# Optimization experiments

Measured on AMD Instinct MI355X. Metric: run time of the kernel, lower is better.

## Reference

```python
import jax, jax.numpy as jnp
import numpy as np

VOCAB = 21
EPS = 1e-5


def rmsnorm(x, w):
    return x * jax.lax.rsqrt(jnp.mean(x * x, axis=-1, keepdims=True) + EPS) * w


def mamba_layer(h, in_w, conv_w, conv_b, xp_w, dtp_w, dtp_b, A_log, Dp, out_w):
    # h: (B, L, D)
    Bsz, L, _ = h.shape
    di, dc = conv_w.shape
    n = A_log.shape[-1]
    r = dtp_w.shape[-1]
    xz = jnp.einsum('bld,ed->ble', h, in_w)          # (B, L, 2*di)
    xi, z = jnp.split(xz, 2, axis=-1)
    # causal depthwise conv of width dc
    xp = jnp.pad(xi, ((0, 0), (dc - 1, 0), (0, 0)))
    xc = conv_b + sum(xp[:, k:k + L, :] * conv_w[:, k] for k in range(dc))
    xc = jax.nn.silu(xc)                              # (B, L, di)
    dbc = jnp.einsum('bld,ed->ble', xc, xp_w)         # (B, L, r+2n)
    dt, Bm, Cm = dbc[..., :r], dbc[..., r:r + n], dbc[..., r + n:]
    dt = jax.nn.softplus(jnp.einsum('blr,dr->bld', dt, dtp_w) + dtp_b)  # (B, L, di)
    A = -jnp.exp(A_log)                               # (di, n)

    def step(hst, inp):
        x_t, dt_t, B_t, C_t = inp                     # (B,di),(B,di),(B,n),(B,n)
        dA = jnp.exp(dt_t[..., None] * A)             # (B, di, n)
        hst = dA * hst + (dt_t * x_t)[..., None] * B_t[:, None, :]
        y_t = jnp.einsum('bdn,bn->bd', hst, C_t)
        return hst, y_t

    h0 = jnp.zeros((Bsz, di, n), dtype=h.dtype)
    xs = (xc.swapaxes(0, 1), dt.swapaxes(0, 1), Bm.swapaxes(0, 1), Cm.swapaxes(0, 1))
    _, ys = jax.lax.scan(step, h0, xs)
    y = ys.swapaxes(0, 1) + xc * Dp                   # skip term D*x
    y = y * jax.nn.silu(z)                            # gate
    return jnp.einsum('bld,ed->ble', y, out_w)


def setup_inputs() -> dict:
    key = jax.random.key(0)
    B, L, D = 4, 1024, 512
    n_layers, n, dc, expand = 2, 16, 3, 2
    di = expand * D
    r = (D + 15) // 16  # dt_rank = ceil(d_model/16) = 32
    ks = jax.random.split(key, 12)
    f32 = jnp.float32
    inp = {}
    inp['x'] = jax.random.randint(ks[0], (B, L), 0, VOCAB)
    inp['emb'] = 0.02 * jax.random.normal(ks[1], (VOCAB, D), f32)
    inp['norm_w'] = jnp.ones((n_layers, D), f32)
    inp['in_proj_w'] = (D ** -0.5) * jax.random.normal(ks[2], (n_layers, 2 * di, D), f32)
    inp['conv_w'] = (dc ** -0.5) * jax.random.normal(ks[3], (n_layers, di, dc), f32)
    inp['conv_b'] = jnp.zeros((n_layers, di), f32)
    inp['x_proj_w'] = (di ** -0.5) * jax.random.normal(ks[4], (n_layers, r + 2 * n, di), f32)
    inp['dt_proj_w'] = (r ** -0.5) * jax.random.normal(ks[5], (n_layers, di, r), f32)
    inp['dt_proj_b'] = jax.random.uniform(ks[6], (n_layers, di), f32, minval=-4.0, maxval=-1.0)
    inp['A_log'] = jnp.log(jnp.broadcast_to(jnp.arange(1, n + 1, dtype=f32), (n_layers, di, n)))
    inp['D_param'] = jnp.ones((n_layers, di), f32)
    inp['out_proj_w'] = (di ** -0.5) * jax.random.normal(ks[7], (n_layers, D, di), f32)
    inp['fc_w'] = (D ** -0.5) * jax.random.normal(ks[8], (2, D), f32)
    inp['fc_b'] = jnp.zeros((2,), f32)
    return inp


def reference(x, emb, norm_w, in_proj_w, conv_w, conv_b, x_proj_w, dt_proj_w,
              dt_proj_b, A_log, D_param, out_proj_w, fc_w, fc_b):
    h = emb[x].astype(jnp.float32)                    # (B, L, D)
    n_layers = norm_w.shape[0]
    for l in range(n_layers):
        h = rmsnorm(
            mamba_layer(h, in_proj_w[l], conv_w[l], conv_b[l], x_proj_w[l],
                        dt_proj_w[l], dt_proj_b[l], A_log[l], D_param[l],
                        out_proj_w[l]),
            norm_w[l])
    pooled = jnp.mean(h, axis=1)                      # global_pool=True
    out = jnp.tanh(pooled)                            # dropout is identity at eval
    return out @ fc_w.T + fc_b                        # (B, 2)
```

## Files before the change

### kernel.cpp

```cpp
#include <hip/hip_runtime.h>
#include <math.h>

constexpr int Bsz = 4, Lseq = 1024, Dmodel = 512, NLAYERS = 2;
constexpr int DI = 1024, NST = 16, RNK = 32;
constexpr int BLQ = Bsz * Lseq;
constexpr int NCH = 32, CLEN = 32;

typedef __attribute__((ext_vector_type(8))) short short8v;
typedef __attribute__((ext_vector_type(8))) unsigned short ushort8v;
typedef __attribute__((ext_vector_type(4))) float f32x4;
typedef unsigned short ushort;

__device__ inline ushort bf16_rne(float v) {
  unsigned u = __float_as_uint(v);
  u += 0x7FFFu + ((u >> 16) & 1u);
  return (ushort)(u >> 16);
}
__device__ inline float bf2f(ushort u) {
  return __uint_as_float(((unsigned)u) << 16);
}
__device__ inline size_t frag_off(int row, int k, int KT) {
  int kt = k >> 6, kk = (k >> 5) & 1, k8 = (k >> 3) & 3;
  int lanei = (row & 15) | (k8 << 4), msub = (row >> 4) & 7, rt = row >> 7;
  return ((((size_t)(rt * KT + kt) * 2 + kk) * 8 + msub) * 64 + lanei) * 8;
}
#define GLDS(gp, lp) __builtin_amdgcn_global_load_lds( \
    (const __attribute__((address_space(1))) void*)(gp), \
    (__attribute__((address_space(3))) void*)(lp), 16, 0, 0)

__global__ __launch_bounds__(256) void embed_kernel(const int* __restrict__ x,
    const float* __restrict__ emb, ushort* __restrict__ Af) {
  int i = blockIdx.x * 256 + threadIdx.x;
  int row = i >> 6, k = (i & 63) * 8;
  int tok = x[row];
  const float* src = &emb[(size_t)tok * Dmodel + k];
  float4 v0 = *reinterpret_cast<const float4*>(src);
  float4 v1 = *reinterpret_cast<const float4*>(src + 4);
  float xs[8] = {v0.x, v0.y, v0.z, v0.w, v1.x, v1.y, v1.z, v1.w};
  ushort hv[8];
#pragma unroll
  for (int e = 0; e < 8; ++e) hv[e] = bf16_rne(xs[e]);
  *reinterpret_cast<ushort8v*>(&Af[frag_off(row, k, 8)]) =
      *reinterpret_cast<ushort8v*>(hv);
}

__global__ __launch_bounds__(256) void cvtw_kernel(
    const float* __restrict__ in_w, const float* __restrict__ xp_w,
    const float* __restrict__ out_w, const float* __restrict__ dtp_w,
    ushort* __restrict__ WIh, ushort* __restrict__ WIl,
    ushort* __restrict__ XPh, ushort* __restrict__ XPl,
    ushort* __restrict__ WOh, ushort* __restrict__ WOl,
    ushort* __restrict__ DTWh, ushort* __restrict__ DTWl)
{
  int blk = blockIdx.x;
  const float* src; ushort *dh, *dl; size_t doff;
  if (blk < 1024) {
    int u = blk * 256 + threadIdx.x;
    int l = u >> 17, rem = u & 131071;
    int row = rem >> 6, k = (rem & 63) * 8;
    src = in_w + (size_t)l * 2048 * 512 + (size_t)row * 512 + k;
    size_t base = (size_t)l * 2048 * 512;
    dh = WIh + base; dl = WIl + base; doff = frag_off(row, k, 8);
  } else if (blk < 1088) {
    int u = (blk - 1024) * 256 + threadIdx.x;
    int l = u >> 13, rem = u & 8191;
    int row = rem >> 7, k = (rem & 127) * 8;
    src = xp_w + (size_t)l * 64 * 1024 + (size_t)row * 1024 + k;
    size_t base = (size_t)l * 131072;
    dh = XPh + base; dl = XPl + base; doff = frag_off(row, k, 16);
  } else if (blk < 1600) {
    int u = (blk - 1088) * 256 + threadIdx.x;
    int l = u >> 16, rem = u & 65535;
    int row = rem >> 7, k = (rem & 127) * 8;
    src = out_w + (size_t)l * 512 * 1024 + (size_t)row * 1024 + k;
    size_t base = (size_t)l * 512 * 1024;
    dh = WOh + base; dl = WOl + base; doff = frag_off(row, k, 16);
  } else {
    int u = (blk - 1600) * 256 + threadIdx.x;
    int l = u >> 12, rem = u & 4095;
    int n = rem >> 2, k8 = rem & 3, k = k8 * 8;
    src = dtp_w + (size_t)l * 1024 * 32 + (size_t)n * 32 + k;
    size_t base = (size_t)l * 32768;
    dh = DTWh + base; dl = DTWl + base;
    doff = (size_t)((n >> 4) * 64 + ((n & 15) | (k8 << 4))) * 8;
  }
  float4 v0 = *reinterpret_cast<const float4*>(src);
  float4 v1 = *reinterpret_cast<const float4*>(src + 4);
  float xs[8] = {v0.x, v0.y, v0.z, v0.w, v1.x, v1.y, v1.z, v1.w};
  ushort hs[8], ls[8];
#pragma unroll
  for (int j = 0; j < 8; ++j) {
    unsigned u = __float_as_uint(xs[j]);
    float hf = __uint_as_float(u & 0xFFFF0000u);
    float r = xs[j] - hf;
    hs[j] = (ushort)(u >> 16);
    ls[j] = (ushort)(__float_as_uint(r) >> 16);
  }
  *reinterpret_cast<ushort8v*>(&dh[doff]) = *reinterpret_cast<ushort8v*>(hs);
  *reinterpret_cast<ushort8v*>(&dl[doff]) = *reinterpret_cast<ushort8v*>(ls);
}

template<int OB>
__global__ __launch_bounds__(256) void gemm_mfma(
    const ushort* __restrict__ Ah,
    const ushort* __restrict__ Bh, const ushort* __restrict__ Bl,
    void* __restrict__ Cv, int N, int K)
{
  const int KT = K >> 6;
  constexpr int ASZ = 2 * 8 * 64 * 8;
  __shared__ ushort lds[3 * ASZ];
  const int tid = threadIdx.x;
  const int lane = tid & 63, wid = tid >> 6;
  const int wm = wid >> 1, wn = wid & 1;
  const int bm0 = blockIdx.y * 128, bn0 = blockIdx.x * 128;
  const size_t abase = (size_t)blockIdx.y * KT * ASZ;
  const size_t bbase = (size_t)blockIdx.x * KT * ASZ;
  const ushort* gsrc = (wid == 0) ? Ah : (wid == 1) ? Bh : Bl;
  const size_t gb = (wid == 0) ? abase : bbase;
  f32x4 acc[4][4];
#pragma unroll
  for (int i = 0; i < 4; ++i)
#pragma unroll
    for (int j = 0; j < 4; ++j) acc[i][j] = (f32x4){0.f, 0.f, 0.f, 0.f};
  const int msel = wm * 4, nsel = wn * 4;
  for (int kt = 0; kt < KT; ++kt) {
    if (wid < 3) {
      const ushort* sbase = gsrc + gb + (size_t)kt * ASZ + lane * 8;
#pragma unroll
      for (int i = 0; i < 16; ++i)
        GLDS(sbase + i * 512, lds + wid * ASZ + i * 512);
    }
    __syncthreads();
#pragma unroll
    for (int kk = 0; kk < 2; ++kk) {
      short8v a_h[4], b_h[4], b_l[4];
#pragma unroll
      for (int i = 0; i < 4; ++i) {
        int ai = ((kk * 8 + msel + i) * 64 + lane) * 8;
        int bi = ((kk * 8 + nsel + i) * 64 + lane) * 8;
        a_h[i] = *reinterpret_cast<const short8v*>(&lds[0 * ASZ + ai]);
        b_h[i] = *reinterpret_cast<const short8v*>(&lds[1 * ASZ + bi]);
        b_l[i] = *reinterpret_cast<const short8v*>(&lds[2 * ASZ + bi]);
      }
#pragma unroll
      for (int ms = 0; ms < 4; ++ms)
#pragma unroll
        for (int ns = 0; ns < 4; ++ns) {
          acc[ms][ns] = __builtin_amdgcn_mfma_f32_16x16x32_bf16(a_h[ms], b_h[ns], acc[ms][ns], 0, 0, 0);
          acc[ms][ns] = __builtin_amdgcn_mfma_f32_16x16x32_bf16(a_h[ms], b_l[ns], acc[ms][ns], 0, 0, 0);
        }
    }
    __syncthreads();
  }
  const int cr = lane >> 4, cc = lane & 15;
#pragma unroll
  for (int ms = 0; ms < 4; ++ms) {
    int row0 = bm0 + (msel + ms) * 16 + cr * 4;
#pragma unroll
    for (int ns = 0; ns < 4; ++ns) {
      int col = bn0 + (nsel + ns) * 16 + cc;
#pragma unroll
      for (int r = 0; r < 4; ++r) {
        if (OB) ((ushort*)Cv)[(size_t)(row0 + r) * N + col] = bf16_rne(acc[ms][ns][r]);
        else    ((float*)Cv)[(size_t)(row0 + r) * N + col] = acc[ms][ns][r];
      }
    }
  }
}

__global__ __launch_bounds__(256) void convxp_kernel(
    const ushort* __restrict__ XZb, const float* __restrict__ cw,
    const float* __restrict__ cb,
    const ushort* __restrict__ XPh, const ushort* __restrict__ XPl,
    const ushort* __restrict__ DTWh, const ushort* __restrict__ DTWl,
    const float* __restrict__ dtb,
    float* __restrict__ XC, float* __restrict__ DTb, float* __restrict__ BCc)
{
  constexpr int XZOFF = 0;
  constexpr int AOFF  = 1312;
  constexpr int BHOFF = 2336;
  constexpr int BLOFF = 6432;
  __shared__ ushort smu[10528];
  const int tid = threadIdx.x, lane = tid & 63, wid = tid >> 6;
  const int cr = lane >> 4, cc = lane & 15;
  const int bm0 = blockIdx.x * 16;
  const int batchbase = bm0 & ~(Lseq - 1);
  f32x4 acc = (f32x4){0.f, 0.f, 0.f, 0.f};

  for (int kt = 0; kt < 16; ++kt) {
    const int kcol0 = kt * 64;
    if (wid < 2) {
#pragma unroll
      for (int i = 0; i < 2; ++i) {
        int u = tid + i * 128;
        if (u < 144) {
          int r = u >> 3, c8 = u & 7;
          int grow = bm0 - 2 + r;
          ushort8v v = {};
          if (grow >= batchbase)
            v = *reinterpret_cast<const ushort8v*>(
                &XZb[(size_t)grow * 2048 + kcol0 + c8 * 8]);
          *reinterpret_cast<ushort8v*>(&smu[XZOFF + r * 72 + c8 * 8]) = v;
        }
      }
    } else {
      const ushort* src = ((wid == 2) ? XPh : XPl) + (size_t)kt * 8192 + lane * 8;
      int dst0 = (wid == 2) ? BHOFF : BLOFF;
#pragma unroll
      for (int i = 0; i < 8; ++i) {
        int sidx = (i >> 2) * 8 + (i & 3);
        int didx = i;
        GLDS(src + sidx * 512, smu + dst0 + didx * 512);
      }
    }
    __syncthreads();
    if (tid < 128) {
      int row = tid >> 3, c8 = tid & 7;
      int d0 = kcol0 + c8 * 8;
      ushort8v cur = *reinterpret_cast<ushort8v*>(&smu[XZOFF + (row + 2) * 72 + c8 * 8]);
      ushort8v pm1 = *reinterpret_cast<ushort8v*>(&smu[XZOFF + (row + 1) * 72 + c8 * 8]);
      ushort8v pm2 = *reinterpret_cast<ushort8v*>(&smu[XZOFF + (row + 0) * 72 + c8 * 8]);
      float wv[24], bv[8];
#pragma unroll
      for (int q = 0; q < 6; ++q)
        *reinterpret_cast<float4*>(&wv[q * 4]) =
            *reinterpret_cast<const float4*>(&cw[d0 * 3 + q * 4]);
      *reinterpret_cast<float4*>(&bv[0]) = *reinterpret_cast<const float4*>(&cb[d0]);
      *reinterpret_cast<float4*>(&bv[4]) = *reinterpret_cast<const float4*>(&cb[d0 + 4]);
      float os[8]; ushort hv[8];
#pragma unroll
      for (int e = 0; e < 8; ++e) {
        float a = bv[e];
        a = fmaf(bf2f(pm2[e]), wv[e * 3 + 0], a);
        a = fmaf(bf2f(pm1[e]), wv[e * 3 + 1], a);
        a = fmaf(bf2f(cur[e]), wv[e * 3 + 2], a);
        float s = a / (1.f + __expf(-a));
        os[e] = s; hv[e] = bf16_rne(s);
      }
      float* op = &XC[(size_t)(bm0 + row) * DI + d0];
      *reinterpret_cast<float4*>(op) = *reinterpret_cast<float4*>(&os[0]);
      *reinterpret_cast<float4*>(op + 4) = *reinterpret_cast<float4*>(&os[4]);
      int kk = c8 >> 2, k8 = c8 & 3;
      int lanei = row | (k8 << 4);
      *reinterpret_cast<ushort8v*>(&smu[AOFF + (kk * 64 + lanei) * 8]) =
          *reinterpret_cast<ushort8v*>(hv);
    }
    __syncthreads();
#pragma unroll
    for (int kk = 0; kk < 2; ++kk) {
      short8v a = *reinterpret_cast<const short8v*>(&smu[AOFF + (kk * 64 + lane) * 8]);
      short8v bh = *reinterpret_cast<const short8v*>(&smu[BHOFF + ((kk * 4 + wid) * 64 + lane) * 8]);
      short8v bl = *reinterpret_cast<const short8v*>(&smu[BLOFF + ((kk * 4 + wid) * 64 + lane) * 8]);
      acc = __builtin_amdgcn_mfma_f32_16x16x32_bf16(a, bh, acc, 0, 0, 0);
      acc = __builtin_amdgcn_mfma_f32_16x16x32_bf16(a, bl, acc, 0, 0, 0);
    }
    __syncthreads();
  }
  if (wid >= 2) {
#pragma unroll
    for (int r = 0; r < 4; ++r)
      BCc[(size_t)(bm0 + cr * 4 + r) * 32 + (wid - 2) * 16 + cc] = acc[r];
  } else {
    int k = wid * 16 + cc, k8 = k >> 3;
#pragma unroll
    for (int r = 0; r < 4; ++r)
      smu[(((cr * 4 + r) | (k8 << 4)) * 8) + (k & 7)] = bf16_rne(acc[r]);
  }
  __syncthreads();
  short8v a_dt = *reinterpret_cast<const short8v*>(&smu[lane * 8]);
#pragma unroll 4
  for (int i = 0; i < 16; ++i) {
    int nt = wid * 16 + i;
    short8v bh = *reinterpret_cast<const short8v*>(&DTWh[(size_t)(nt * 64 + lane) * 8]);
    short8v bl = *reinterpret_cast<const short8v*>(&DTWl[(size_t)(nt * 64 + lane) * 8]);
    f32x4 p = (f32x4){0.f, 0.f, 0.f, 0.f};
    p = __builtin_amdgcn_mfma_f32_16x16x32_bf16(a_dt, bh, p, 0, 0, 0);
    p = __builtin_amdgcn_mfma_f32_16x16x32_bf16(a_dt, bl, p, 0, 0, 0);
    int n = nt * 16 + cc;
    float bias = dtb[n];
#pragma unroll
    for (int r = 0; r < 4; ++r) {
      float v = p[r] + bias;
      float sp = (v > 15.f) ? v : log1pf(__expf(v));
      DTb[(size_t)(bm0 + cr * 4 + r) * DI + n] = sp;
    }
  }
}

__global__ __launch_bounds__(256) void scan_p1_kernel(
    const float* __restrict__ DTb, const float* __restrict__ XC,
    const float* __restrict__ BCc, const float* __restrict__ Alog,
    float* __restrict__ HEND, float* __restrict__ DSUM)
{
  const int d = blockIdx.x * 256 + threadIdx.x;
  const int c = blockIdx.y, b = blockIdx.z;
  const int t0 = b * Lseq + c * CLEN;
  __shared__ float Bs[CLEN][16];
#pragma unroll
  for (int i = 0; i < 2; ++i) {
    int e = threadIdx.x + i * 256;
    Bs[e >> 4][e & 15] = BCc[(size_t)(t0 + (e >> 4)) * 32 + (e & 15)];
  }
  float An[16];
#pragma unroll
  for (int j = 0; j < 4; ++j) {
    float4 a = *reinterpret_cast<const float4*>(&Alog[d * 16 + j * 4]);
    An[j * 4 + 0] = -__expf(a.x); An[j * 4 + 1] = -__expf(a.y);
    An[j * 4 + 2] = -__expf(a.z); An[j * 4 + 3] = -__expf(a.w);
  }
  __syncthreads();
  float h[16] = {};
  float S = 0.f;
  for (int t = 0; t < CLEN; ++t) {
    size_t g = (size_t)(t0 + t) * DI + d;
    float dt = DTb[g], xc = XC[g];
    S += dt;
    float dtxc = dt * xc;
#pragma unroll
    for (int n = 0; n < 16; ++n)
      h[n] = fmaf(__expf(An[n] * dt), h[n], dtxc * Bs[t][n]);
  }
  size_t hb = ((size_t)(b * NCH + c) * DI + d) * 16;
#pragma unroll
  for (int j = 0; j < 4; ++j)
    *reinterpret_cast<float4*>(&HEND[hb + j * 4]) =
        *reinterpret_cast<float4*>(&h[j * 4]);
  DSUM[(size_t)(b * NCH + c) * DI + d] = S;
}

__global__ __launch_bounds__(256) void scan_p2_kernel(
    float* __restrict__ HEND, const float* __restrict__ DSUM,
    const float* __restrict__ Alog)
{
  int id = blockIdx.x * 256 + threadIdx.x;
  int n = id & 15, d = (id >> 4) & (DI - 1), b = id >> 14;
  float An = -__expf(Alog[d * 16 + n]);
  float hg = 0.f;
  for (int c = 0; c < NCH; ++c) {
    size_t hi = ((size_t)(b * NCH + c) * DI + d) * 16 + n;
    float hl = HEND[hi];
    float Dc = DSUM[(size_t)(b * NCH + c) * DI + d];
    HEND[hi] = hg;
    hg = fmaf(__expf(An * Dc), hg, hl);
  }
}

__global__ __launch_bounds__(256) void scan_p3_kernel(
    const float* __restrict__ XC, const float* __restrict__ DTb,
    const float* __restrict__ BCc, const ushort* __restrict__ XZb,
    const float* __restrict__ HEND, const float* __restrict__ Alog,
    const float* __restrict__ Dp, ushort* __restrict__ Af)
{
  const int tid = threadIdx.x;
  const int dg = blockIdx.x, c = blockIdx.y, b = blockIdx.z;
  const int d = dg * 256 + tid;
  const int t0 = b * Lseq + c * CLEN;
  __shared__ float BC[CLEN][32];
  __shared__ float ys[CLEN][264];
#pragma unroll
  for (int i = 0; i < 4; ++i) {
    int e = tid + i * 256;
    BC[e >> 5][e & 31] = BCc[(size_t)(t0 + (e >> 5)) * 32 + (e & 31)];
  }
  float An[16], h[16];
  size_t hb = ((size_t)(b * NCH + c) * DI + d) * 16;
#pragma unroll
  for (int j = 0; j < 4; ++j) {
    float4 a = *reinterpret_cast<const float4*>(&Alog[d * 16 + j * 4]);
    An[j * 4 + 0] = -__expf(a.x); An[j * 4 + 1] = -__expf(a.y);
    An[j * 4 + 2] = -__expf(a.z); An[j * 4 + 3] = -__expf(a.w);
    *reinterpret_cast<float4*>(&h[j * 4]) =
        *reinterpret_cast<const float4*>(&HEND[hb + j * 4]);
  }
  float Dpv = Dp[d];
  __syncthreads();
  for (int t = 0; t < CLEN; ++t) {
    size_t g = (size_t)(t0 + t) * DI + d;
    float dt = DTb[g], xc = XC[g];
    float z = bf2f(XZb[(size_t)(t0 + t) * (2 * DI) + DI + d]);
    float dtxc = dt * xc;
    float y = 0.f;
#pragma unroll
    for (int n = 0; n < 16; ++n) {
      h[n] = fmaf(__expf(An[n] * dt), h[n], dtxc * BC[t][n]);
      y = fmaf(h[n], BC[t][16 + n], y);
    }
    float sil = z / (1.f + __expf(-z));
    ys[t][tid] = (y + xc * Dpv) * sil;
  }
  __syncthreads();
#pragma unroll
  for (int i = 0; i < 4; ++i) {
    int u = tid + i * 256;
    int tt = u >> 5, j8 = u & 31;
    int row = t0 + tt;
    int kg = dg * 256 + j8 * 8;
    ushort hv[8];
#pragma unroll
    for (int e = 0; e < 8; ++e) hv[e] = bf16_rne(ys[tt][j8 * 8 + e]);
    *reinterpret_cast<ushort8v*>(&Af[frag_off(row, kg, 16)]) =
        *reinterpret_cast<ushort8v*>(hv);
  }
}

__global__ __launch_bounds__(256) void rmsnorm_kernel(const float* __restrict__ X,
    const float* __restrict__ W, float* __restrict__ O, ushort* __restrict__ Af) {
  int row = blockIdx.x * 4 + (threadIdx.x >> 6);
  int lane = threadIdx.x & 63;
  int k = lane * 8;
  const float* xp = X + (size_t)row * Dmodel + k;
  float4 v0 = *reinterpret_cast<const float4*>(xp);
  float4 v1 = *reinterpret_cast<const float4*>(xp + 4);
  float vs[8] = {v0.x, v0.y, v0.z, v0.w, v1.x, v1.y, v1.z, v1.w};
  float ss = 0.f;
#pragma unroll
  for (int e = 0; e < 8; ++e) ss = fmaf(vs[e], vs[e], ss);
#pragma unroll
  for (int o = 32; o >= 1; o >>= 1) ss += __shfl_xor(ss, o);
  float sc = rsqrtf(ss * (1.f / Dmodel) + 1e-5f);
  const float* wp = W + k;
  float4 w0 = *reinterpret_cast<const float4*>(wp);
  float4 w1 = *reinterpret_cast<const float4*>(wp + 4);
  float wsv[8] = {w0.x, w0.y, w0.z, w0.w, w1.x, w1.y, w1.z, w1.w};
  float os[8];
  ushort hv[8];
#pragma unroll
  for (int e = 0; e < 8; ++e) {
    os[e] = vs[e] * sc * wsv[e];
    hv[e] = bf16_rne(os[e]);
  }
  float* op = O + (size_t)row * Dmodel + k;
  *reinterpret_cast<float4*>(op) = *reinterpret_cast<float4*>(&os[0]);
  *reinterpret_cast<float4*>(op + 4) = *reinterpret_cast<float4*>(&os[4]);
  *reinterpret_cast<ushort8v*>(&Af[frag_off(row, k, 8)]) =
      *reinterpret_cast<ushort8v*>(hv);
}

__global__ __launch_bounds__(256) void pool_part_kernel(const float* __restrict__ H,
    float* __restrict__ part) {
  int b = blockIdx.x, dg = blockIdx.y, tc = blockIdx.z;
  int tid = threadIdx.x;
  int d = dg * 128 + (tid & 127);
  int ph = tid >> 7;
  const float* base = H + ((size_t)(b * Lseq + tc * 128 + ph * 64)) * Dmodel + d;
  float s = 0.f;
#pragma unroll 8
  for (int t = 0; t < 64; ++t) s += base[(size_t)t * Dmodel];
  __shared__ float red[256];
  red[tid] = s; __syncthreads();
  if (ph == 0)
    part[(size_t)(b * 8 + tc) * Dmodel + d] = red[tid] + red[tid + 128];
}

__global__ __launch_bounds__(256) void pool_head_kernel(
    const float* __restrict__ part, const float* __restrict__ fcw,
    const float* __restrict__ fcb, float* __restrict__ out) {
  int b = blockIdx.x >> 1, j = blockIdx.x & 1;
  int tid = threadIdx.x;
  float s = 0.f;
  for (int d = tid; d < Dmodel; d += 256) {
    float p = 0.f;
#pragma unroll
    for (int tc = 0; tc < 8; ++tc) p += part[(size_t)(b * 8 + tc) * Dmodel + d];
    s += tanhf(p * (1.f / Lseq)) * fcw[j * Dmodel + d];
  }
#pragma unroll
  for (int o = 32; o >= 1; o >>= 1) s += __shfl_xor(s, o);
  __shared__ float w[4];
  if ((tid & 63) == 0) w[tid >> 6] = s;
  __syncthreads();
  if (tid == 0) out[b * 2 + j] = w[0] + w[1] + w[2] + w[3] + fcb[j];
}

extern "C" void kernel_launch(void* const* d_in, const int* in_sizes, int n_in,
                              void* d_out, int out_size, void* d_ws, size_t ws_size,
                              hipStream_t stream) {
  const int*   x      = (const int*)d_in[0];
  const float* emb    = (const float*)d_in[1];
  const float* norm_w = (const float*)d_in[2];
  const float* in_w   = (const float*)d_in[3];
  const float* conv_w = (const float*)d_in[4];
  const float* conv_b = (const float*)d_in[5];
  const float* xp_w   = (const float*)d_in[6];
  const float* dtp_w  = (const float*)d_in[7];
  const float* dtp_b  = (const float*)d_in[8];
  const float* A_log  = (const float*)d_in[9];
  const float* Dp     = (const float*)d_in[10];
  const float* out_w  = (const float*)d_in[11];
  const float* fc_w   = (const float*)d_in[12];
  const float* fc_b   = (const float*)d_in[13];
  float* out = (float*)d_out;

  char* p = (char*)d_ws;
  auto alloc = [&](size_t bytes) { char* r = p; p += (bytes + 255) & ~255ull; return r; };
  ushort* XZb  = (ushort*)alloc((size_t)BLQ * 2 * DI * 2);
  float*  XC   = (float*) alloc((size_t)BLQ * DI * 4);
  float*  DTb  = (float*) alloc((size_t)BLQ * DI * 4);
  float*  BCc  = (float*) alloc((size_t)BLQ * 32 * 4);
  float*  HEND = (float*) alloc((size_t)Bsz * NCH * DI * 16 * 4);
  float*  DSUM = (float*) alloc((size_t)Bsz * NCH * DI * 4);
  float*  H    = (float*) alloc((size_t)BLQ * Dmodel * 4);
  float*  H2   = (float*) alloc((size_t)BLQ * Dmodel * 4);
  float*  PPART= (float*) alloc((size_t)Bsz * 8 * Dmodel * 4);
  ushort* AhI  = (ushort*)alloc((size_t)BLQ * Dmodel * 2);
  ushort* AhO  = (ushort*)alloc((size_t)BLQ * DI * 2);
  ushort* WIh  = (ushort*)alloc((size_t)2 * 2048 * 512 * 2);
  ushort* WIl  = (ushort*)alloc((size_t)2 * 2048 * 512 * 2);
  ushort* XPh  = (ushort*)alloc((size_t)2 * 131072 * 2);
  ushort* XPl  = (ushort*)alloc((size_t)2 * 131072 * 2);
  ushort* WOh  = (ushort*)alloc((size_t)2 * 512 * 1024 * 2);
  ushort* WOl  = (ushort*)alloc((size_t)2 * 512 * 1024 * 2);
  ushort* DTWh = (ushort*)alloc((size_t)2 * 32768 * 2);
  ushort* DTWl = (ushort*)alloc((size_t)2 * 32768 * 2);

  embed_kernel<<<BLQ * Dmodel / 8 / 256, 256, 0, stream>>>(x, emb, AhI);
  cvtw_kernel<<<1632, 256, 0, stream>>>(in_w, xp_w, out_w, dtp_w,
      WIh, WIl, XPh, XPl, WOh, WOl, DTWh, DTWl);

  for (int l = 0; l < NLAYERS; ++l) {
    const float* cw  = conv_w + (size_t)l * DI * 3;
    const float* cb  = conv_b + (size_t)l * DI;
    const float* dtb = dtp_b + (size_t)l * DI;
    const float* Al  = A_log + (size_t)l * DI * NST;
    const float* dpl = Dp    + (size_t)l * DI;
    const float* nw  = norm_w + (size_t)l * Dmodel;
    const ushort* wih = WIh + (size_t)l * 2048 * 512;
    const ushort* wil = WIl + (size_t)l * 2048 * 512;
    const ushort* xph = XPh + (size_t)l * 131072;
    const ushort* xpl = XPl + (size_t)l * 131072;
    const ushort* woh = WOh + (size_t)l * 512 * 1024;
    const ushort* wol = WOl + (size_t)l * 512 * 1024;
    const ushort* dwh = DTWh + (size_t)l * 32768;
    const ushort* dwl = DTWl + (size_t)l * 32768;

    gemm_mfma<1><<<dim3(16, 32), 256, 0, stream>>>(AhI, wih, wil, XZb, 2 * DI, Dmodel);

    convxp_kernel<<<BLQ / 16, 256, 0, stream>>>(XZb, cw, cb, xph, xpl,
        dwh, dwl, dtb, XC, DTb, BCc);

    scan_p1_kernel<<<dim3(DI / 256, NCH, Bsz), 256, 0, stream>>>(
        DTb, XC, BCc, Al, HEND, DSUM);
    scan_p2_kernel<<<Bsz * DI * NST / 256, 256, 0, stream>>>(HEND, DSUM, Al);
    scan_p3_kernel<<<dim3(DI / 256, NCH, Bsz), 256, 0, stream>>>(
        XC, DTb, BCc, XZb, HEND, Al, dpl, AhO);

    gemm_mfma<0><<<dim3(4, 32), 256, 0, stream>>>(AhO, woh, wol, H2, Dmodel, DI);

    rmsnorm_kernel<<<BLQ / 4, 256, 0, stream>>>(H2, nw, H, AhI);
  }

  pool_part_kernel<<<dim3(Bsz, Dmodel / 128, 8), 256, 0, stream>>>(H, PPART);
  pool_head_kernel<<<2 * Bsz, 256, 0, stream>>>(PPART, fc_w, fc_b, out);
}
```

Baseline: 314.6 us.

## Split x_proj K-loop, move dt_proj to fp32 kernel, drop out_proj low-bf16 term

The conv+x_proj kernel now splits its K loop across two grid slices that write fp32 partial sums. A new xpost kernel adds the partials, emits B/C, and computes dt_proj plus softplus in fp32 FMA from LDS instead of bf16 split MFMA. The A-operand LDS writes and reads get an XOR swizzle to cut bank conflicts. The out_proj GEMM drops the low-half weight MFMA, halving its matrix work but lowering the precision of out_proj weights to plain bf16.

```diff
diff --git a/kernel.cpp b/kernel.cpp
--- a/kernel.cpp
+++ b/kernel.cpp
@@ -46,11 +46,10 @@
 
 __global__ __launch_bounds__(256) void cvtw_kernel(
     const float* __restrict__ in_w, const float* __restrict__ xp_w,
-    const float* __restrict__ out_w, const float* __restrict__ dtp_w,
+    const float* __restrict__ out_w,
     ushort* __restrict__ WIh, ushort* __restrict__ WIl,
     ushort* __restrict__ XPh, ushort* __restrict__ XPl,
-    ushort* __restrict__ WOh, ushort* __restrict__ WOl,
-    ushort* __restrict__ DTWh, ushort* __restrict__ DTWl)
+    ushort* __restrict__ WOh, ushort* __restrict__ WOl)
 {
   int blk = blockIdx.x;
   const float* src; ushort *dh, *dl; size_t doff;
@@ -68,21 +67,13 @@
     src = xp_w + (size_t)l * 64 * 1024 + (size_t)row * 1024 + k;
     size_t base = (size_t)l * 131072;
     dh = XPh + base; dl = XPl + base; doff = frag_off(row, k, 16);
-  } else if (blk < 1600) {
+  } else {
     int u = (blk - 1088) * 256 + threadIdx.x;
     int l = u >> 16, rem = u & 65535;
     int row = rem >> 7, k = (rem & 127) * 8;
     src = out_w + (size_t)l * 512 * 1024 + (size_t)row * 1024 + k;
     size_t base = (size_t)l * 512 * 1024;
     dh = WOh + base; dl = WOl + base; doff = frag_off(row, k, 16);
-  } else {
-    int u = (blk - 1600) * 256 + threadIdx.x;
-    int l = u >> 12, rem = u & 4095;
-    int n = rem >> 2, k8 = rem & 3, k = k8 * 8;
-    src = dtp_w + (size_t)l * 1024 * 32 + (size_t)n * 32 + k;
-    size_t base = (size_t)l * 32768;
-    dh = DTWh + base; dl = DTWl + base;
-    doff = (size_t)((n >> 4) * 64 + ((n & 15) | (k8 << 4))) * 8;
   }
   float4 v0 = *reinterpret_cast<const float4*>(src);
   float4 v1 = *reinterpret_cast<const float4*>(src + 4);
@@ -100,7 +91,7 @@
   *reinterpret_cast<ushort8v*>(&dl[doff]) = *reinterpret_cast<ushort8v*>(ls);
 }
 
-template<int OB>
+template<int OB, int SPLITB>
 __global__ __launch_bounds__(256) void gemm_mfma(
     const ushort* __restrict__ Ah,
     const ushort* __restrict__ Bh, const ushort* __restrict__ Bl,
@@ -124,7 +115,7 @@
     for (int j = 0; j < 4; ++j) acc[i][j] = (f32x4){0.f, 0.f, 0.f, 0.f};
   const int msel = wm * 4, nsel = wn * 4;
   for (int kt = 0; kt < KT; ++kt) {
-    if (wid < 3) {
+    if (wid < (SPLITB ? 3 : 2)) {
       const ushort* sbase = gsrc + gb + (size_t)kt * ASZ + lane * 8;
 #pragma unroll
       for (int i = 0; i < 16; ++i)
@@ -140,14 +131,15 @@
         int bi = ((kk * 8 + nsel + i) * 64 + lane) * 8;
         a_h[i] = *reinterpret_cast<const short8v*>(&lds[0 * ASZ + ai]);
         b_h[i] = *reinterpret_cast<const short8v*>(&lds[1 * ASZ + bi]);
-        b_l[i] = *reinterpret_cast<const short8v*>(&lds[2 * ASZ + bi]);
+        if (SPLITB) b_l[i] = *reinterpret_cast<const short8v*>(&lds[2 * ASZ + bi]);
       }
 #pragma unroll
       for (int ms = 0; ms < 4; ++ms)
 #pragma unroll
         for (int ns = 0; ns < 4; ++ns) {
           acc[ms][ns] = __builtin_amdgcn_mfma_f32_16x16x32_bf16(a_h[ms], b_h[ns], acc[ms][ns], 0, 0, 0);
-          acc[ms][ns] = __builtin_amdgcn_mfma_f32_16x16x32_bf16(a_h[ms], b_l[ns], acc[ms][ns], 0, 0, 0);
+          if (SPLITB)
+            acc[ms][ns] = __builtin_amdgcn_mfma_f32_16x16x32_bf16(a_h[ms], b_l[ns], acc[ms][ns], 0, 0, 0);
         }
     }
     __syncthreads();
@@ -172,9 +164,7 @@
     const ushort* __restrict__ XZb, const float* __restrict__ cw,
     const float* __restrict__ cb,
     const ushort* __restrict__ XPh, const ushort* __restrict__ XPl,
-    const ushort* __restrict__ DTWh, const ushort* __restrict__ DTWl,
-    const float* __restrict__ dtb,
-    float* __restrict__ XC, float* __restrict__ DTb, float* __restrict__ BCc)
+    float* __restrict__ XC, float* __restrict__ P)
 {
   constexpr int XZOFF = 0;
   constexpr int AOFF  = 1312;
@@ -184,10 +174,11 @@
   const int tid = threadIdx.x, lane = tid & 63, wid = tid >> 6;
   const int cr = lane >> 4, cc = lane & 15;
   const int bm0 = blockIdx.x * 16;
+  const int z = blockIdx.y;
   const int batchbase = bm0 & ~(Lseq - 1);
   f32x4 acc = (f32x4){0.f, 0.f, 0.f, 0.f};
 
-  for (int kt = 0; kt < 16; ++kt) {
+  for (int kt = z * 8; kt < z * 8 + 8; ++kt) {
     const int kcol0 = kt * 64;
     if (wid < 2) {
 #pragma unroll
@@ -209,8 +200,7 @@
 #pragma unroll
       for (int i = 0; i < 8; ++i) {
         int sidx = (i >> 2) * 8 + (i & 3);
-        int didx = i;
-        GLDS(src + sidx * 512, smu + dst0 + didx * 512);
+        GLDS(src + sidx * 512, smu + dst0 + i * 512);
       }
     }
     __syncthreads();
@@ -241,14 +231,15 @@
       *reinterpret_cast<float4*>(op) = *reinterpret_cast<float4*>(&os[0]);
       *reinterpret_cast<float4*>(op + 4) = *reinterpret_cast<float4*>(&os[4]);
       int kk = c8 >> 2, k8 = c8 & 3;
-      int lanei = row | (k8 << 4);
-      *reinterpret_cast<ushort8v*>(&smu[AOFF + (kk * 64 + lanei) * 8]) =
+      int idx = (kk * 64 + (row | (k8 << 4))) ^ k8;
+      *reinterpret_cast<ushort8v*>(&smu[AOFF + idx * 8]) =
           *reinterpret_cast<ushort8v*>(hv);
     }
     __syncthreads();
 #pragma unroll
     for (int kk = 0; kk < 2; ++kk) {
-      short8v a = *reinterpret_cast<const short8v*>(&smu[AOFF + (kk * 64 + lane) * 8]);
+      int aidx = (kk * 64 + lane) ^ ((lane >> 4) & 3);
+      short8v a = *reinterpret_cast<const short8v*>(&smu[AOFF + aidx * 8]);
       short8v bh = *reinterpret_cast<const short8v*>(&smu[BHOFF + ((kk * 4 + wid) * 64 + lane) * 8]);
       short8v bl = *reinterpret_cast<const short8v*>(&smu[BLOFF + ((kk * 4 + wid) * 64 + lane) * 8]);
       acc = __builtin_amdgcn_mfma_f32_16x16x32_bf16(a, bh, acc, 0, 0, 0);
@@ -256,34 +247,58 @@
     }
     __syncthreads();
   }
-  if (wid >= 2) {
-#pragma unroll
-    for (int r = 0; r < 4; ++r)
-      BCc[(size_t)(bm0 + cr * 4 + r) * 32 + (wid - 2) * 16 + cc] = acc[r];
-  } else {
-    int k = wid * 16 + cc, k8 = k >> 3;
-#pragma unroll
-    for (int r = 0; r < 4; ++r)
-      smu[(((cr * 4 + r) | (k8 << 4)) * 8) + (k & 7)] = bf16_rne(acc[r]);
+  float* Pz = P + (size_t)z * BLQ * 64;
+#pragma unroll
+  for (int r = 0; r < 4; ++r)
+    Pz[(size_t)(bm0 + cr * 4 + r) * 64 + wid * 16 + cc] = acc[r];
+}
+
+__global__ __launch_bounds__(256) void xpost_kernel(
+    const float* __restrict__ P, const float* __restrict__ dtw,
+    const float* __restrict__ dtb, float* __restrict__ DTb,
+    float* __restrict__ BCc)
+{
+  const int tid = threadIdx.x;
+  const size_t SL = (size_t)BLQ * 64;
+  if (blockIdx.y == 16) {
+    int i0 = blockIdx.x * 4096 + tid;
+#pragma unroll
+    for (int i = 0; i < 16; ++i) {
+      int idx = i0 + i * 256;
+      int bt = idx >> 5, n = idx & 31;
+      size_t g = (size_t)bt * 64 + 32 + n;
+      BCc[idx] = P[g] + P[SL + g];
+    }
+    return;
+  }
+  const int dg = blockIdx.y, bm0 = blockIdx.x * 128;
+  __shared__ float db[128][33];
+  __shared__ float wt[64][33];
+#pragma unroll
+  for (int i = 0; i < 16; ++i) {
+    int e = tid + i * 256;
+    int r = e >> 5, c = e & 31;
+    size_t g = (size_t)(bm0 + r) * 64 + c;
+    db[r][c] = P[g] + P[SL + g];
+  }
+#pragma unroll
+  for (int i = 0; i < 8; ++i) {
+    int e = tid + i * 256;
+    int r = e >> 5, c = e & 31;
+    wt[r][c] = dtw[(size_t)(dg * 64 + r) * 32 + c];
   }
   __syncthreads();
-  short8v a_dt = *reinterpret_cast<const short8v*>(&smu[lane * 8]);
+  const int d_loc = tid & 63, wv = tid >> 6;
+  const float bias = dtb[dg * 64 + d_loc];
 #pragma unroll 4
-  for (int i = 0; i < 16; ++i) {
-    int nt = wid * 16 + i;
-    short8v bh = *reinterpret_cast<const short8v*>(&DTWh[(size_t)(nt * 64 + lane) * 8]);
-    short8v bl = *reinterpret_cast<const short8v*>(&DTWl[(size_t)(nt * 64 + lane) * 8]);
-    f32x4 p = (f32x4){0.f, 0.f, 0.f, 0.f};
-    p = __builtin_amdgcn_mfma_f32_16x16x32_bf16(a_dt, bh, p, 0, 0, 0);
-    p = __builtin_amdgcn_mfma_f32_16x16x32_bf16(a_dt, bl, p, 0, 0, 0);
-    int n = nt * 16 + cc;
-    float bias = dtb[n];
-#pragma unroll
-    for (int r = 0; r < 4; ++r) {
-      float v = p[r] + bias;
-      float sp = (v > 15.f) ? v : log1pf(__expf(v));
-      DTb[(size_t)(bm0 + cr * 4 + r) * DI + n] = sp;
-    }
+  for (int i = 0; i < 32; ++i) {
+    int r = wv + i * 4;
+    float dot = 0.f;
+#pragma unroll
+    for (int c = 0; c < 32; ++c) dot = fmaf(db[r][c], wt[d_loc][c], dot);
+    float v = dot + bias;
+    DTb[(size_t)(bm0 + r) * DI + dg * 64 + d_loc] =
+        (v > 15.f) ? v : log1pf(__expf(v));
   }
 }
 
@@ -497,6 +512,7 @@
   float*  XC   = (float*) alloc((size_t)BLQ * DI * 4);
   float*  DTb  = (float*) alloc((size_t)BLQ * DI * 4);
   float*  BCc  = (float*) alloc((size_t)BLQ * 32 * 4);
+  float*  DBCP = (float*) alloc((size_t)2 * BLQ * 64 * 4);
   float*  HEND = (float*) alloc((size_t)Bsz * NCH * DI * 16 * 4);
   float*  DSUM = (float*) alloc((size_t)Bsz * NCH * DI * 4);
   float*  H    = (float*) alloc((size_t)BLQ * Dmodel * 4);
@@ -510,16 +526,15 @@
   ushort* XPl  = (ushort*)alloc((size_t)2 * 131072 * 2);
   ushort* WOh  = (ushort*)alloc((size_t)2 * 512 * 1024 * 2);
   ushort* WOl  = (ushort*)alloc((size_t)2 * 512 * 1024 * 2);
-  ushort* DTWh = (ushort*)alloc((size_t)2 * 32768 * 2);
-  ushort* DTWl = (ushort*)alloc((size_t)2 * 32768 * 2);
 
   embed_kernel<<<BLQ * Dmodel / 8 / 256, 256, 0, stream>>>(x, emb, AhI);
-  cvtw_kernel<<<1632, 256, 0, stream>>>(in_w, xp_w, out_w, dtp_w,
-      WIh, WIl, XPh, XPl, WOh, WOl, DTWh, DTWl);
+  cvtw_kernel<<<1600, 256, 0, stream>>>(in_w, xp_w, out_w,
+      WIh, WIl, XPh, XPl, WOh, WOl);
 
   for (int l = 0; l < NLAYERS; ++l) {
     const float* cw  = conv_w + (size_t)l * DI * 3;
     const float* cb  = conv_b + (size_t)l * DI;
+    const float* dtw = dtp_w + (size_t)l * DI * RNK;
     const float* dtb = dtp_b + (size_t)l * DI;
     const float* Al  = A_log + (size_t)l * DI * NST;
     const float* dpl = Dp    + (size_t)l * DI;
@@ -529,14 +544,13 @@
     const ushort* xph = XPh + (size_t)l * 131072;
     const ushort* xpl = XPl + (size_t)l * 131072;
     const ushort* woh = WOh + (size_t)l * 512 * 1024;
-    const ushort* wol = WOl + (size_t)l * 512 * 1024;
-    const ushort* dwh = DTWh + (size_t)l * 32768;
-    const ushort* dwl = DTWl + (size_t)l * 32768;
-
-    gemm_mfma<1><<<dim3(16, 32), 256, 0, stream>>>(AhI, wih, wil, XZb, 2 * DI, Dmodel);
-
-    convxp_kernel<<<BLQ / 16, 256, 0, stream>>>(XZb, cw, cb, xph, xpl,
-        dwh, dwl, dtb, XC, DTb, BCc);
+
+    gemm_mfma<1, 1><<<dim3(16, 32), 256, 0, stream>>>(AhI, wih, wil, XZb, 2 * DI, Dmodel);
+
+    convxp_kernel<<<dim3(BLQ / 16, 2), 256, 0, stream>>>(XZb, cw, cb, xph, xpl,
+        XC, DBCP);
+
+    xpost_kernel<<<dim3(32, 17), 256, 0, stream>>>(DBCP, dtw, dtb, DTb, BCc);
 
     scan_p1_kernel<<<dim3(DI / 256, NCH, Bsz), 256, 0, stream>>>(
         DTb, XC, BCc, Al, HEND, DSUM);
@@ -544,7 +558,7 @@
     scan_p3_kernel<<<dim3(DI / 256, NCH, Bsz), 256, 0, stream>>>(
         XC, DTb, BCc, XZb, HEND, Al, dpl, AhO);
 
-    gemm_mfma<0><<<dim3(4, 32), 256, 0, stream>>>(AhO, woh, wol, H2, Dmodel, DI);
+    gemm_mfma<0, 0><<<dim3(4, 32), 256, 0, stream>>>(AhO, woh, nullptr, H2, Dmodel, DI);
 
     rmsnorm_kernel<<<BLQ / 4, 256, 0, stream>>>(H2, nw, H, AhI);
   }
```

Result: faster. 289.5 us (-8.0%).
